# Optimization experiments

Hardware: AMD Instinct MI355X
Metric: run time of the kernel (lower is better)

The kernel has to match this reference:

```python
import jax, jax.numpy as jnp
import numpy as np

N = 500_000          # num nodes
K = 3                # neighbors per star subgraph = graphlet_size - 1
E = N * K            # one subgraph per node -> directed (center, nbr) edges
L = 2                # hop_neighbor
FD = 2               # final_dim = 2**pqc_dim
H = 64               # hidden_dim
NC = 8               # num_classes
NIN = 16             # node_input_dim
EIN = 8              # edge_input_dim


def _lin(k, i, o):
    # torch.nn.Linear-style init scale
    return jax.random.normal(k, (i, o), jnp.float32) * (1.0 / np.sqrt(i))


def setup_inputs() -> dict:
    key = jax.random.key(0)
    ks = jax.random.split(key, 32)
    node_feat = jax.random.normal(ks[0], (N, NIN), jnp.float32)
    edge_attr = jax.random.normal(ks[1], (E, EIN), jnp.float32)
    # edge e = (center, neighbor); centers grouped: edges 3i..3i+2 belong to node i
    centers = jnp.repeat(jnp.arange(N, dtype=jnp.int32), K)
    neighbors = jax.random.randint(ks[2], (E,), 0, N, dtype=jnp.int32)
    edge_index = jnp.stack([centers, neighbors])  # [2, E]
    batch = jnp.zeros((N,), jnp.int32)
    msg_W1 = jnp.stack([_lin(ks[6 + i], 2 * FD, H) for i in range(L)])
    msg_W2 = jnp.stack([_lin(ks[8 + i], H, FD) for i in range(L)])
    upd_W1 = jnp.stack([_lin(ks[10 + i], 2 * FD, H) for i in range(L)])
    upd_W2 = jnp.stack([_lin(ks[12 + i], H, FD) for i in range(L)])
    return dict(
        node_feat=node_feat, edge_attr=edge_attr, edge_index=edge_index, batch=batch,
        Wn=_lin(ks[3], NIN, FD), bn=jnp.zeros((FD,), jnp.float32),
        We=_lin(ks[4], EIN, FD), be=jnp.zeros((FD,), jnp.float32),
        msg_W1=msg_W1, msg_b1=jnp.zeros((L, H), jnp.float32),
        msg_W2=msg_W2, msg_b2=jnp.zeros((L, FD), jnp.float32),
        upd_W1=upd_W1, upd_b1=jnp.zeros((L, H), jnp.float32),
        upd_W2=upd_W2, upd_b2=jnp.zeros((L, FD), jnp.float32),
        fin_W1=_lin(ks[14], FD, H), fin_b1=jnp.zeros((H,), jnp.float32),
        fin_W2=_lin(ks[15], H, NC), fin_b2=jnp.zeros((NC,), jnp.float32),
    )


def _leaky(x):
    return jnp.where(x >= 0, x, 0.1 * x)


def _mlp(x, W1, b1, W2, b2):
    # MLP([din, 64, dout], act=LeakyReLU(0.1)); dropout inactive at eval
    return _leaky(x @ W1 + b1) @ W2 + b2


def reference(node_feat, edge_attr, edge_index, batch, Wn, bn, We, be,
              msg_W1, msg_b1, msg_W2, msg_b2, upd_W1, upd_b1, upd_W2, upd_b2,
              fin_W1, fin_b1, fin_W2, fin_b2):
    ctr = edge_index[0]  # [E] center of each star edge
    nbr = edge_index[1]  # [E] neighbor
    h = node_feat @ Wn + bn      # [N, FD] input_node projection
    e = edge_attr @ We + be      # [E, FD] input_edge projection (fixed across layers)
    for l in range(L):
        # message over each (center, neighbor) edge: concat(edge_feat, nbr_feat)
        msg = _mlp(jnp.concatenate([e, h[nbr]], axis=1),
                   msg_W1[l], msg_b1[l], msg_W2[l], msg_b2[l])  # [E, FD]
        aggr = jax.ops.segment_sum(msg, ctr, num_segments=N)    # [N, FD]
        new = _mlp(jnp.concatenate([h, aggr], axis=1),
                   upd_W1[l], upd_b1[l], upd_W2[l], upd_b2[l])  # [N, FD]
        h = jax.nn.relu(h + new)  # updates_node[center] += new_center; then ReLU
    return _mlp(h, fin_W1, fin_b1, fin_W2, fin_b2)  # [N, NC]
```

## Files before the change

kernel.cpp:

```cpp
#include <hip/hip_runtime.h>

#define NN 500000
#define KK 3
#define EE (NN * KK)
#define HH 64
#define NC 8
#define NIN 16
#define EIN 8

typedef __attribute__((ext_vector_type(2))) _Float16 h2;
typedef __attribute__((ext_vector_type(2)))  float sf2;
typedef __attribute__((ext_vector_type(8)))  float sf8;
typedef __attribute__((ext_vector_type(16))) float sf16;

using pk_t = decltype(__builtin_amdgcn_cvt_pkrtz(0.f, 0.f));

__device__ __forceinline__ sf2 sload2(const float* p) {
    sf2 r; asm("s_load_dwordx2 %0, %1, 0x0" : "=s"(r) : "s"(p)); return r;
}
__device__ __forceinline__ sf8 sload8(const float* p) {
    sf8 r; asm("s_load_dwordx8 %0, %1, 0x0" : "=s"(r) : "s"(p)); return r;
}
__device__ __forceinline__ sf16 sload16(const float* p) {
    sf16 r; asm("s_load_dwordx16 %0, %1, 0x0" : "=s"(r) : "s"(p)); return r;
}
#define SWAIT1(a)         asm volatile("s_waitcnt lgkmcnt(0)" : "+s"(a))
#define SWAIT2(a,b)       asm volatile("s_waitcnt lgkmcnt(0)" : "+s"(a),"+s"(b))
#define SWAIT3(a,b,c)     asm volatile("s_waitcnt lgkmcnt(0)" : "+s"(a),"+s"(b),"+s"(c))
#define SWAIT4(a,b,c,d)   asm volatile("s_waitcnt lgkmcnt(0)" : "+s"(a),"+s"(b),"+s"(c),"+s"(d))
#define SWAIT5(a,b,c,d,e) asm volatile("s_waitcnt lgkmcnt(0)" : "+s"(a),"+s"(b),"+s"(c),"+s"(d),"+s"(e))

#if __has_builtin(__builtin_elementwise_fma)
#define PKFMA(a,b,c) __builtin_elementwise_fma((a),(b),(c))
#else
#define PKFMA(a,b,c) ((a)*(b)+(c))
#endif

__device__ __forceinline__ h2 bch2(float f)        { return __builtin_bit_cast(h2, f); }
__device__ __forceinline__ h2 bch2u(unsigned int u){ return __builtin_bit_cast(h2, u); }
__device__ __forceinline__ h2 dup16(float f) {
    return __builtin_bit_cast(h2, __builtin_amdgcn_cvt_pkrtz(f, f));
}
__device__ __forceinline__ unsigned int pkrtz_u(float a, float b) {
    return __builtin_bit_cast(unsigned int, __builtin_amdgcn_cvt_pkrtz(a, b));
}
__device__ __forceinline__ h2 splat_lo(unsigned int u) {
    h2 p = bch2u(u); h2 r; r.x = p.x; r.y = p.x; return r;
}
__device__ __forceinline__ h2 splat_hi(unsigned int u) {
    h2 p = bch2u(u); h2 r; r.x = p.y; r.y = p.y; return r;
}
__device__ __forceinline__ float lo_f32(unsigned int u) { return (float)bch2u(u).x; }
__device__ __forceinline__ float hi_f32(unsigned int u) { return (float)bch2u(u).y; }

__device__ __forceinline__ float fdot2(h2 a, h2 b, float c) {
#if __has_builtin(__builtin_amdgcn_fdot2)
    return __builtin_amdgcn_fdot2(__builtin_bit_cast(pk_t, a),
                                  __builtin_bit_cast(pk_t, b), c, false);
#else
    return c + (float)a.x * (float)b.x + (float)a.y * (float)b.y;
#endif
}
__device__ __forceinline__ h2 lk2(h2 x) {
    h2 c = {(_Float16)0.1f, (_Float16)0.1f};
    return __builtin_elementwise_max(x, x * c);
}
__device__ __forceinline__ float pack2(float a, float b) {
    h2 v; v.x = (_Float16)a; v.y = (_Float16)b;
    return __builtin_bit_cast(float, v);
}

__global__ __launch_bounds__(256) void prep_kernel(
    const float* __restrict__ node_feat, const float* __restrict__ edge_attr,
    const float* __restrict__ Wn, const float* __restrict__ bn,
    const float* __restrict__ We, const float* __restrict__ be,
    unsigned int* __restrict__ hp, unsigned int* __restrict__ ep,
    const float* __restrict__ msgW1, const float* __restrict__ msgb1, const float* __restrict__ msgW2,
    const float* __restrict__ updW1, const float* __restrict__ updb1, const float* __restrict__ updW2,
    const float* __restrict__ finW1, const float* __restrict__ finb1, const float* __restrict__ finW2,
    float* __restrict__ wpack)
{
    sf16 wn0 = sload16(Wn);
    sf16 wn1 = sload16(Wn + 16);
    sf2  bnv = sload2(bn);
    sf16 wev = sload16(We);
    sf2  bev = sload2(be);
    SWAIT5(wn0, wn1, bnv, wev, bev);

    int idx = blockIdx.x * 256 + threadIdx.x;
    if (idx < NN) {
        const float4* x4 = (const float4*)(node_feat + (size_t)idx * NIN);
        float4 v0 = x4[0], v1 = x4[1], v2 = x4[2], v3 = x4[3];
        float xs[16] = {v0.x, v0.y, v0.z, v0.w, v1.x, v1.y, v1.z, v1.w,
                        v2.x, v2.y, v2.z, v2.w, v3.x, v3.y, v3.z, v3.w};
        float a0 = bnv.x, a1 = bnv.y;
#pragma unroll
        for (int i = 0; i < 8; i++) {
            a0 = fmaf(xs[i], wn0[2 * i], a0);
            a1 = fmaf(xs[i], wn0[2 * i + 1], a1);
        }
#pragma unroll
        for (int i = 0; i < 8; i++) {
            a0 = fmaf(xs[8 + i], wn1[2 * i], a0);
            a1 = fmaf(xs[8 + i], wn1[2 * i + 1], a1);
        }
        hp[idx] = pkrtz_u(a0, a1);
    } else if (idx < NN + EE) {
        int eidx = idx - NN;
        const float4* x4 = (const float4*)(edge_attr + (size_t)eidx * EIN);
        float4 v0 = x4[0], v1 = x4[1];
        float xs[8] = {v0.x, v0.y, v0.z, v0.w, v1.x, v1.y, v1.z, v1.w};
        float a0 = bev.x, a1 = bev.y;
#pragma unroll
        for (int i = 0; i < 8; i++) {
            a0 = fmaf(xs[i], wev[2 * i], a0);
            a1 = fmaf(xs[i], wev[2 * i + 1], a1);
        }
        ep[eidx] = pkrtz_u(a0, a1);
    }

    if (blockIdx.x == 0) {
        int t = threadIdx.x;
        if (t < 32) {
            int l = t >> 4, which = (t >> 3) & 1, c = t & 7;
            const float* W1 = (which ? updW1 : msgW1) + l * 4 * HH;
            const float* b1 = (which ? updb1 : msgb1) + l * HH;
            const float* W2 = (which ? updW2 : msgW2) + l * 2 * HH;
            float* dst = wpack + (l * 2 + which) * 256 + c * 32;
            int j0 = c * 8;
            for (int r = 0; r < 4; r++)
                for (int p = 0; p < 4; p++)
                    dst[r * 4 + p] = pack2(W1[r * HH + j0 + 2 * p], W1[r * HH + j0 + 2 * p + 1]);
            for (int p = 0; p < 4; p++) {
                dst[16 + p] = pack2(b1[j0 + 2 * p], b1[j0 + 2 * p + 1]);
                dst[20 + p] = pack2(W2[(j0 + 2 * p) * 2 + 0], W2[(j0 + 2 * p + 1) * 2 + 0]);
                dst[24 + p] = pack2(W2[(j0 + 2 * p) * 2 + 1], W2[(j0 + 2 * p + 1) * 2 + 1]);
                dst[28 + p] = 0.0f;
            }
        } else if (t < 40) {
            int c = t - 32, j0 = c * 8;
            float* dst = wpack + 1024 + c * 48;
            for (int p = 0; p < 4; p++) {
                dst[p]      = pack2(finW1[j0 + 2 * p],      finW1[j0 + 2 * p + 1]);
                dst[4 + p]  = pack2(finW1[HH + j0 + 2 * p], finW1[HH + j0 + 2 * p + 1]);
                dst[8 + p]  = pack2(finb1[j0 + 2 * p],      finb1[j0 + 2 * p + 1]);
                dst[12 + p] = 0.0f;
            }
            for (int jp = 0; jp < 4; jp++)
                for (int cc = 0; cc < NC; cc++)
                    dst[16 + jp * 8 + cc] = pack2(finW2[(j0 + 2 * jp) * NC + cc],
                                                  finW2[(j0 + 2 * jp + 1) * NC + cc]);
        }
    }
}

template<bool FINAL>
__global__ __launch_bounds__(256) void layer_kernel(
    const unsigned int* __restrict__ hp_in, const unsigned int* __restrict__ eP,
    const int* __restrict__ nbr,
    const float* __restrict__ mblk, const float* __restrict__ mb2,
    const float* __restrict__ ublk, const float* __restrict__ ub2,
    unsigned int* __restrict__ hp_out,
    const float* __restrict__ fblk, const float* __restrict__ fb2,
    float* __restrict__ out)
{
    int i = blockIdx.x * 256 + threadIdx.x;
    if (i >= NN) return;

    sf2 mb2v = sload2(mb2);
    sf2 ub2v = sload2(ub2);
    SWAIT2(mb2v, ub2v);

    unsigned int hO = hp_in[i];
    int base = i * KK;
    int n0 = nbr[base + 0], n1 = nbr[base + 1], n2 = nbr[base + 2];
    unsigned int g0 = hp_in[n0], g1 = hp_in[n1], g2 = hp_in[n2];
    unsigned int e0 = eP[base + 0], e1 = eP[base + 1], e2 = eP[base + 2];

    h2 e0x = splat_lo(e0), e0y = splat_hi(e0);
    h2 e1x = splat_lo(e1), e1y = splat_hi(e1);
    h2 e2x = splat_lo(e2), e2y = splat_hi(e2);
    h2 n0x = splat_lo(g0), n0y = splat_hi(g0);
    h2 n1x = splat_lo(g1), n1y = splat_hi(g1);
    h2 n2x = splat_lo(g2), n2y = splat_hi(g2);

    float a0 = 3.0f * mb2v.x, a1 = 3.0f * mb2v.y;
#pragma unroll 1
    for (int c = 0; c < 8; c += 2) {
        sf16 A0 = sload16(mblk + c * 32);
        sf16 B0 = sload16(mblk + c * 32 + 16);
        sf16 A1 = sload16(mblk + c * 32 + 32);
        sf16 B1 = sload16(mblk + c * 32 + 48);
        SWAIT4(A0, B0, A1, B1);
#pragma unroll
        for (int half = 0; half < 2; half++) {
            const sf16& A = half ? A1 : A0;
            const sf16& B = half ? B1 : B0;
#pragma unroll
            for (int jp = 0; jp < 4; jp++) {
                h2 w0 = bch2(A[jp]), w1 = bch2(A[4 + jp]);
                h2 w2 = bch2(A[8 + jp]), w3 = bch2(A[12 + jp]);
                h2 bb = bch2(B[jp]);
                h2 t0 = PKFMA(e0x, w0, PKFMA(e0y, w1, PKFMA(n0x, w2, PKFMA(n0y, w3, bb))));
                h2 t1 = PKFMA(e1x, w0, PKFMA(e1y, w1, PKFMA(n1x, w2, PKFMA(n1y, w3, bb))));
                h2 t2 = PKFMA(e2x, w0, PKFMA(e2y, w1, PKFMA(n2x, w2, PKFMA(n2y, w3, bb))));
                h2 ts = lk2(t0) + lk2(t1) + lk2(t2);
                a0 = fdot2(ts, bch2(B[4 + jp]), a0);
                a1 = fdot2(ts, bch2(B[8 + jp]), a1);
            }
        }
    }

    h2 hx = splat_lo(hO), hy = splat_hi(hO);
    h2 ax = dup16(a0), ay = dup16(a1);
    float u0 = ub2v.x, u1 = ub2v.y;
#pragma unroll 1
    for (int c = 0; c < 8; c += 2) {
        sf16 A0 = sload16(ublk + c * 32);
        sf16 B0 = sload16(ublk + c * 32 + 16);
        sf16 A1 = sload16(ublk + c * 32 + 32);
        sf16 B1 = sload16(ublk + c * 32 + 48);
        SWAIT4(A0, B0, A1, B1);
#pragma unroll
        for (int half = 0; half < 2; half++) {
            const sf16& A = half ? A1 : A0;
            const sf16& B = half ? B1 : B0;
#pragma unroll
            for (int jp = 0; jp < 4; jp++) {
                h2 tt = PKFMA(hx, bch2(A[jp]),
                        PKFMA(hy, bch2(A[4 + jp]),
                        PKFMA(ax, bch2(A[8 + jp]),
                        PKFMA(ay, bch2(A[12 + jp]), bch2(B[jp])))));
                tt = lk2(tt);
                u0 = fdot2(tt, bch2(B[4 + jp]), u0);
                u1 = fdot2(tt, bch2(B[8 + jp]), u1);
            }
        }
    }
    float nh0 = fmaxf(lo_f32(hO) + u0, 0.0f);
    float nh1 = fmaxf(hi_f32(hO) + u1, 0.0f);

    if constexpr (!FINAL) {
        hp_out[i] = pkrtz_u(nh0, nh1);
    } else {
        sf8 fb2v = sload8(fb2);
        SWAIT1(fb2v);
        float o[NC];
#pragma unroll
        for (int cc = 0; cc < NC; cc++) o[cc] = fb2v[cc];
        h2 nx = dup16(nh0), ny = dup16(nh1);
#pragma unroll 1
        for (int c = 0; c < 8; c++) {
            sf16 A = sload16(fblk + c * 48);
            sf16 B = sload16(fblk + c * 48 + 16);
            sf16 C = sload16(fblk + c * 48 + 32);
            SWAIT3(A, B, C);
#pragma unroll
            for (int jp = 0; jp < 4; jp++) {
                h2 w1a = bch2(A[jp]), w1b = bch2(A[4 + jp]), bb = bch2(A[8 + jp]);
                h2 tt = lk2(PKFMA(nx, w1a, PKFMA(ny, w1b, bb)));
#pragma unroll
                for (int cc = 0; cc < NC; cc++) {
                    float w = (jp < 2) ? B[(jp & 1) * 8 + cc] : C[(jp & 1) * 8 + cc];
                    o[cc] = fdot2(tt, bch2(w), o[cc]);
                }
            }
        }
        float4* op = (float4*)(out + (size_t)i * NC);
        op[0] = make_float4(o[0], o[1], o[2], o[3]);
        op[1] = make_float4(o[4], o[5], o[6], o[7]);
    }
}

extern "C" void kernel_launch(void* const* d_in, const int* in_sizes, int n_in,
                              void* d_out, int out_size, void* d_ws, size_t ws_size,
                              hipStream_t stream) {
    const float* node_feat = (const float*)d_in[0];
    const float* edge_attr = (const float*)d_in[1];
    const int* edge_index = (const int*)d_in[2];
    const float* Wn = (const float*)d_in[4];
    const float* bn = (const float*)d_in[5];
    const float* We = (const float*)d_in[6];
    const float* be = (const float*)d_in[7];
    const float* msgW1 = (const float*)d_in[8];
    const float* msgb1 = (const float*)d_in[9];
    const float* msgW2 = (const float*)d_in[10];
    const float* msgb2 = (const float*)d_in[11];
    const float* updW1 = (const float*)d_in[12];
    const float* updb1 = (const float*)d_in[13];
    const float* updW2 = (const float*)d_in[14];
    const float* updb2 = (const float*)d_in[15];
    const float* finW1 = (const float*)d_in[16];
    const float* finb1 = (const float*)d_in[17];
    const float* finW2 = (const float*)d_in[18];
    const float* finb2 = (const float*)d_in[19];
    float* out = (float*)d_out;

    const int* nbr = edge_index + EE;

    char* ws = (char*)d_ws;
    unsigned int* hA = (unsigned int*)ws;
    unsigned int* hB = (unsigned int*)(ws + (size_t)NN * 4);
    unsigned int* eP = (unsigned int*)(ws + (size_t)NN * 8);
    float* wpack = (float*)(ws + (size_t)NN * 8 + (size_t)EE * 4);

    const int threads = 256;
    int prep_grid = (NN + EE + threads - 1) / threads;
    prep_kernel<<<prep_grid, threads, 0, stream>>>(
        node_feat, edge_attr, Wn, bn, We, be, hA, eP,
        msgW1, msgb1, msgW2, updW1, updb1, updW2,
        finW1, finb1, finW2, wpack);

    int grid = (NN + threads - 1) / threads;
    layer_kernel<false><<<grid, threads, 0, stream>>>(
        hA, eP, nbr,
        wpack + 0 * 256, msgb2,
        wpack + 1 * 256, updb2,
        hB, wpack + 1024, finb2, nullptr);
    layer_kernel<true><<<grid, threads, 0, stream>>>(
        hB, eP, nbr,
        wpack + 2 * 256, msgb2 + 2,
        wpack + 3 * 256, updb2 + 2,
        nullptr, wpack + 1024, finb2, out);
}
```

Baseline: 197.4 us.

## Fuse input projections into first layer, recomputing neighbor projections

Drops the separate prep kernel and merges the node and edge input projections into the first message-passing layer. Each thread gathers raw 16-float node features for its three neighbors and re-projects them instead of reading a precomputed packed h, and it runs layer-1 MLPs in fp32. This removes one launch and the round trip of the projected h through memory. In exchange it gathers 64-byte rows instead of 4-byte ones for random neighbors and does more fp32 ALU work. Weight packing for layer 2 and the final MLP moves into block 0 of the fused kernel.

```diff
diff --git a/kernel.cpp b/kernel.cpp
--- a/kernel.cpp
+++ b/kernel.cpp
@@ -24,11 +24,11 @@
 __device__ __forceinline__ sf16 sload16(const float* p) {
     sf16 r; asm("s_load_dwordx16 %0, %1, 0x0" : "=s"(r) : "s"(p)); return r;
 }
-#define SWAIT1(a)         asm volatile("s_waitcnt lgkmcnt(0)" : "+s"(a))
-#define SWAIT2(a,b)       asm volatile("s_waitcnt lgkmcnt(0)" : "+s"(a),"+s"(b))
-#define SWAIT3(a,b,c)     asm volatile("s_waitcnt lgkmcnt(0)" : "+s"(a),"+s"(b),"+s"(c))
-#define SWAIT4(a,b,c,d)   asm volatile("s_waitcnt lgkmcnt(0)" : "+s"(a),"+s"(b),"+s"(c),"+s"(d))
-#define SWAIT5(a,b,c,d,e) asm volatile("s_waitcnt lgkmcnt(0)" : "+s"(a),"+s"(b),"+s"(c),"+s"(d),"+s"(e))
+#define SWAIT1(a)           asm volatile("s_waitcnt lgkmcnt(0)" : "+s"(a))
+#define SWAIT2(a,b)         asm volatile("s_waitcnt lgkmcnt(0)" : "+s"(a),"+s"(b))
+#define SWAIT3(a,b,c)       asm volatile("s_waitcnt lgkmcnt(0)" : "+s"(a),"+s"(b),"+s"(c))
+#define SWAIT5(a,b,c,d,e)   asm volatile("s_waitcnt lgkmcnt(0)" : "+s"(a),"+s"(b),"+s"(c),"+s"(d),"+s"(e))
+#define SWAIT6(a,b,c,d,e,f) asm volatile("s_waitcnt lgkmcnt(0)" : "+s"(a),"+s"(b),"+s"(c),"+s"(d),"+s"(e),"+s"(f))
 
 #if __has_builtin(__builtin_elementwise_fma)
 #define PKFMA(a,b,c) __builtin_elementwise_fma((a),(b),(c))
@@ -61,6 +61,7 @@
     return c + (float)a.x * (float)b.x + (float)a.y * (float)b.y;
 #endif
 }
+__device__ __forceinline__ float lky(float x)  { return fmaxf(x, 0.1f * x); }
 __device__ __forceinline__ h2 lk2(h2 x) {
     h2 c = {(_Float16)0.1f, (_Float16)0.1f};
     return __builtin_elementwise_max(x, x * c);
@@ -70,63 +71,44 @@
     return __builtin_bit_cast(float, v);
 }
 
-__global__ __launch_bounds__(256) void prep_kernel(
-    const float* __restrict__ node_feat, const float* __restrict__ edge_attr,
-    const float* __restrict__ Wn, const float* __restrict__ bn,
-    const float* __restrict__ We, const float* __restrict__ be,
-    unsigned int* __restrict__ hp, unsigned int* __restrict__ ep,
-    const float* __restrict__ msgW1, const float* __restrict__ msgb1, const float* __restrict__ msgW2,
-    const float* __restrict__ updW1, const float* __restrict__ updb1, const float* __restrict__ updW2,
-    const float* __restrict__ finW1, const float* __restrict__ finb1, const float* __restrict__ finW2,
-    float* __restrict__ wpack)
-{
-    sf16 wn0 = sload16(Wn);
-    sf16 wn1 = sload16(Wn + 16);
-    sf2  bnv = sload2(bn);
-    sf16 wev = sload16(We);
-    sf2  bev = sload2(be);
-    SWAIT5(wn0, wn1, bnv, wev, bev);
-
-    int idx = blockIdx.x * 256 + threadIdx.x;
-    if (idx < NN) {
-        const float4* x4 = (const float4*)(node_feat + (size_t)idx * NIN);
-        float4 v0 = x4[0], v1 = x4[1], v2 = x4[2], v3 = x4[3];
-        float xs[16] = {v0.x, v0.y, v0.z, v0.w, v1.x, v1.y, v1.z, v1.w,
-                        v2.x, v2.y, v2.z, v2.w, v3.x, v3.y, v3.z, v3.w};
-        float a0 = bnv.x, a1 = bnv.y;
-#pragma unroll
-        for (int i = 0; i < 8; i++) {
-            a0 = fmaf(xs[i], wn0[2 * i], a0);
-            a1 = fmaf(xs[i], wn0[2 * i + 1], a1);
-        }
-#pragma unroll
-        for (int i = 0; i < 8; i++) {
-            a0 = fmaf(xs[8 + i], wn1[2 * i], a0);
-            a1 = fmaf(xs[8 + i], wn1[2 * i + 1], a1);
-        }
-        hp[idx] = pkrtz_u(a0, a1);
-    } else if (idx < NN + EE) {
-        int eidx = idx - NN;
-        const float4* x4 = (const float4*)(edge_attr + (size_t)eidx * EIN);
-        float4 v0 = x4[0], v1 = x4[1];
-        float xs[8] = {v0.x, v0.y, v0.z, v0.w, v1.x, v1.y, v1.z, v1.w};
-        float a0 = bev.x, a1 = bev.y;
-#pragma unroll
-        for (int i = 0; i < 8; i++) {
-            a0 = fmaf(xs[i], wev[2 * i], a0);
-            a1 = fmaf(xs[i], wev[2 * i + 1], a1);
-        }
-        ep[eidx] = pkrtz_u(a0, a1);
-    }
-
+struct P1 {
+    const float *node_feat, *edge_attr; const int* nbr;
+    const float *Wn, *bn, *We, *be;
+    const float *mW1, *mb1, *mW2, *mb2, *uW1, *ub1, *uW2, *ub2;
+    const float *mW1p, *uW1p, *mb1p, *ub1p, *mW2p, *uW2p;
+    const float *fW1, *fb1, *fW2;
+    unsigned int *hp, *ep; float* wpack;
+};
+
+__device__ __forceinline__ float2 projN(const float* node_feat, int idx,
+                                        const sf16& wn0, const sf16& wn1, const sf2& bnv) {
+    const float4* x4 = (const float4*)(node_feat + (size_t)idx * NIN);
+    float4 v0 = x4[0], v1 = x4[1], v2 = x4[2], v3 = x4[3];
+    float xs[16] = {v0.x, v0.y, v0.z, v0.w, v1.x, v1.y, v1.z, v1.w,
+                    v2.x, v2.y, v2.z, v2.w, v3.x, v3.y, v3.z, v3.w};
+    float a0 = bnv.x, a1 = bnv.y;
+#pragma unroll
+    for (int i = 0; i < 8; i++) {
+        a0 = fmaf(xs[i], wn0[2 * i], a0);
+        a1 = fmaf(xs[i], wn0[2 * i + 1], a1);
+    }
+#pragma unroll
+    for (int i = 0; i < 8; i++) {
+        a0 = fmaf(xs[8 + i], wn1[2 * i], a0);
+        a1 = fmaf(xs[8 + i], wn1[2 * i + 1], a1);
+    }
+    return make_float2(a0, a1);
+}
+
+__global__ __launch_bounds__(256) void k1_kernel(P1 P) {
     if (blockIdx.x == 0) {
         int t = threadIdx.x;
-        if (t < 32) {
-            int l = t >> 4, which = (t >> 3) & 1, c = t & 7;
-            const float* W1 = (which ? updW1 : msgW1) + l * 4 * HH;
-            const float* b1 = (which ? updb1 : msgb1) + l * HH;
-            const float* W2 = (which ? updW2 : msgW2) + l * 2 * HH;
-            float* dst = wpack + (l * 2 + which) * 256 + c * 32;
+        if (t < 16) {
+            int which = t >> 3, c = t & 7;
+            const float* W1 = which ? P.uW1p : P.mW1p;
+            const float* b1 = which ? P.ub1p : P.mb1p;
+            const float* W2 = which ? P.uW2p : P.mW2p;
+            float* dst = P.wpack + (2 + which) * 256 + c * 32;
             int j0 = c * 8;
             for (int r = 0; r < 4; r++)
                 for (int p = 0; p < 4; p++)
@@ -137,30 +119,109 @@
                 dst[24 + p] = pack2(W2[(j0 + 2 * p) * 2 + 1], W2[(j0 + 2 * p + 1) * 2 + 1]);
                 dst[28 + p] = 0.0f;
             }
-        } else if (t < 40) {
-            int c = t - 32, j0 = c * 8;
-            float* dst = wpack + 1024 + c * 48;
+        } else if (t < 24) {
+            int c = t - 16, j0 = c * 8;
+            float* dst = P.wpack + 1024 + c * 48;
             for (int p = 0; p < 4; p++) {
-                dst[p]      = pack2(finW1[j0 + 2 * p],      finW1[j0 + 2 * p + 1]);
-                dst[4 + p]  = pack2(finW1[HH + j0 + 2 * p], finW1[HH + j0 + 2 * p + 1]);
-                dst[8 + p]  = pack2(finb1[j0 + 2 * p],      finb1[j0 + 2 * p + 1]);
+                dst[p]      = pack2(P.fW1[j0 + 2 * p],      P.fW1[j0 + 2 * p + 1]);
+                dst[4 + p]  = pack2(P.fW1[HH + j0 + 2 * p], P.fW1[HH + j0 + 2 * p + 1]);
+                dst[8 + p]  = pack2(P.fb1[j0 + 2 * p],      P.fb1[j0 + 2 * p + 1]);
                 dst[12 + p] = 0.0f;
             }
             for (int jp = 0; jp < 4; jp++)
                 for (int cc = 0; cc < NC; cc++)
-                    dst[16 + jp * 8 + cc] = pack2(finW2[(j0 + 2 * jp) * NC + cc],
-                                                  finW2[(j0 + 2 * jp + 1) * NC + cc]);
-        }
-    }
-}
-
-template<bool FINAL>
-__global__ __launch_bounds__(256) void layer_kernel(
+                    dst[16 + jp * 8 + cc] = pack2(P.fW2[(j0 + 2 * jp) * NC + cc],
+                                                  P.fW2[(j0 + 2 * jp + 1) * NC + cc]);
+        }
+    }
+
+    int i = blockIdx.x * 256 + threadIdx.x;
+    if (i >= NN) return;
+
+    sf16 wn0 = sload16(P.Wn);
+    sf16 wn1 = sload16(P.Wn + 16);
+    sf2  bnv = sload2(P.bn);
+    sf16 wev = sload16(P.We);
+    sf2  bev = sload2(P.be);
+    SWAIT5(wn0, wn1, bnv, wev, bev);
+
+    int base = i * KK;
+    int n0 = P.nbr[base + 0], n1 = P.nbr[base + 1], n2 = P.nbr[base + 2];
+
+    float2 hh = projN(P.node_feat, i,  wn0, wn1, bnv);
+    float2 g0 = projN(P.node_feat, n0, wn0, wn1, bnv);
+    float2 g1 = projN(P.node_feat, n1, wn0, wn1, bnv);
+    float2 g2 = projN(P.node_feat, n2, wn0, wn1, bnv);
+
+    float ex[3], ey[3];
+#pragma unroll
+    for (int k = 0; k < 3; k++) {
+        const float4* x4 = (const float4*)(P.edge_attr + (size_t)(base + k) * EIN);
+        float4 v0 = x4[0], v1 = x4[1];
+        float xs[8] = {v0.x, v0.y, v0.z, v0.w, v1.x, v1.y, v1.z, v1.w};
+        float a0 = bev.x, a1 = bev.y;
+#pragma unroll
+        for (int q = 0; q < 8; q++) {
+            a0 = fmaf(xs[q], wev[2 * q], a0);
+            a1 = fmaf(xs[q], wev[2 * q + 1], a1);
+        }
+        ex[k] = a0; ey[k] = a1;
+        P.ep[base + k] = pkrtz_u(a0, a1);
+    }
+
+    sf2 mb2v = sload2(P.mb2);
+    sf2 ub2v = sload2(P.ub2);
+    SWAIT2(mb2v, ub2v);
+
+    float a0 = 3.0f * mb2v.x, a1 = 3.0f * mb2v.y;
+#pragma unroll 1
+    for (int j0 = 0; j0 < HH; j0 += 8) {
+        sf8 w0 = sload8(P.mW1 + j0);
+        sf8 w1 = sload8(P.mW1 + HH + j0);
+        sf8 w2 = sload8(P.mW1 + 2 * HH + j0);
+        sf8 w3 = sload8(P.mW1 + 3 * HH + j0);
+        sf8 bb = sload8(P.mb1 + j0);
+        sf16 wc = sload16(P.mW2 + 2 * j0);
+        SWAIT6(w0, w1, w2, w3, bb, wc);
+#pragma unroll
+        for (int q = 0; q < 8; q++) {
+            float t0 = fmaf(ex[0], w0[q], fmaf(ey[0], w1[q], fmaf(g0.x, w2[q], fmaf(g0.y, w3[q], bb[q]))));
+            float t1 = fmaf(ex[1], w0[q], fmaf(ey[1], w1[q], fmaf(g1.x, w2[q], fmaf(g1.y, w3[q], bb[q]))));
+            float t2 = fmaf(ex[2], w0[q], fmaf(ey[2], w1[q], fmaf(g2.x, w2[q], fmaf(g2.y, w3[q], bb[q]))));
+            float ts = lky(t0) + lky(t1) + lky(t2);
+            a0 = fmaf(ts, wc[2 * q], a0);
+            a1 = fmaf(ts, wc[2 * q + 1], a1);
+        }
+    }
+
+    float u0 = ub2v.x, u1 = ub2v.y;
+#pragma unroll 1
+    for (int j0 = 0; j0 < HH; j0 += 8) {
+        sf8 w0 = sload8(P.uW1 + j0);
+        sf8 w1 = sload8(P.uW1 + HH + j0);
+        sf8 w2 = sload8(P.uW1 + 2 * HH + j0);
+        sf8 w3 = sload8(P.uW1 + 3 * HH + j0);
+        sf8 bb = sload8(P.ub1 + j0);
+        sf16 wc = sload16(P.uW2 + 2 * j0);
+        SWAIT6(w0, w1, w2, w3, bb, wc);
+#pragma unroll
+        for (int q = 0; q < 8; q++) {
+            float tt = fmaf(hh.x, w0[q], fmaf(hh.y, w1[q], fmaf(a0, w2[q], fmaf(a1, w3[q], bb[q]))));
+            tt = lky(tt);
+            u0 = fmaf(tt, wc[2 * q], u0);
+            u1 = fmaf(tt, wc[2 * q + 1], u1);
+        }
+    }
+    float nh0 = fmaxf(hh.x + u0, 0.0f);
+    float nh1 = fmaxf(hh.y + u1, 0.0f);
+    P.hp[i] = pkrtz_u(nh0, nh1);
+}
+
+__global__ __launch_bounds__(256) void k2_kernel(
     const unsigned int* __restrict__ hp_in, const unsigned int* __restrict__ eP,
     const int* __restrict__ nbr,
     const float* __restrict__ mblk, const float* __restrict__ mb2,
     const float* __restrict__ ublk, const float* __restrict__ ub2,
-    unsigned int* __restrict__ hp_out,
     const float* __restrict__ fblk, const float* __restrict__ fb2,
     float* __restrict__ out)
 {
@@ -191,7 +252,7 @@
         sf16 B0 = sload16(mblk + c * 32 + 16);
         sf16 A1 = sload16(mblk + c * 32 + 32);
         sf16 B1 = sload16(mblk + c * 32 + 48);
-        SWAIT4(A0, B0, A1, B1);
+        asm volatile("s_waitcnt lgkmcnt(0)" : "+s"(A0), "+s"(B0), "+s"(A1), "+s"(B1));
 #pragma unroll
         for (int half = 0; half < 2; half++) {
             const sf16& A = half ? A1 : A0;
@@ -220,7 +281,7 @@
         sf16 B0 = sload16(ublk + c * 32 + 16);
         sf16 A1 = sload16(ublk + c * 32 + 32);
         sf16 B1 = sload16(ublk + c * 32 + 48);
-        SWAIT4(A0, B0, A1, B1);
+        asm volatile("s_waitcnt lgkmcnt(0)" : "+s"(A0), "+s"(B0), "+s"(A1), "+s"(B1));
 #pragma unroll
         for (int half = 0; half < 2; half++) {
             const sf16& A = half ? A1 : A0;
@@ -240,36 +301,32 @@
     float nh0 = fmaxf(lo_f32(hO) + u0, 0.0f);
     float nh1 = fmaxf(hi_f32(hO) + u1, 0.0f);
 
-    if constexpr (!FINAL) {
-        hp_out[i] = pkrtz_u(nh0, nh1);
-    } else {
-        sf8 fb2v = sload8(fb2);
-        SWAIT1(fb2v);
-        float o[NC];
-#pragma unroll
-        for (int cc = 0; cc < NC; cc++) o[cc] = fb2v[cc];
-        h2 nx = dup16(nh0), ny = dup16(nh1);
-#pragma unroll 1
-        for (int c = 0; c < 8; c++) {
-            sf16 A = sload16(fblk + c * 48);
-            sf16 B = sload16(fblk + c * 48 + 16);
-            sf16 C = sload16(fblk + c * 48 + 32);
-            SWAIT3(A, B, C);
-#pragma unroll
-            for (int jp = 0; jp < 4; jp++) {
-                h2 w1a = bch2(A[jp]), w1b = bch2(A[4 + jp]), bb = bch2(A[8 + jp]);
-                h2 tt = lk2(PKFMA(nx, w1a, PKFMA(ny, w1b, bb)));
-#pragma unroll
-                for (int cc = 0; cc < NC; cc++) {
-                    float w = (jp < 2) ? B[(jp & 1) * 8 + cc] : C[(jp & 1) * 8 + cc];
-                    o[cc] = fdot2(tt, bch2(w), o[cc]);
-                }
-            }
-        }
-        float4* op = (float4*)(out + (size_t)i * NC);
-        op[0] = make_float4(o[0], o[1], o[2], o[3]);
-        op[1] = make_float4(o[4], o[5], o[6], o[7]);
-    }
+    sf8 fb2v = sload8(fb2);
+    SWAIT1(fb2v);
+    float o[NC];
+#pragma unroll
+    for (int cc = 0; cc < NC; cc++) o[cc] = fb2v[cc];
+    h2 nx = dup16(nh0), ny = dup16(nh1);
+#pragma unroll 1
+    for (int c = 0; c < 8; c++) {
+        sf16 A = sload16(fblk + c * 48);
+        sf16 B = sload16(fblk + c * 48 + 16);
+        sf16 C = sload16(fblk + c * 48 + 32);
+        SWAIT3(A, B, C);
+#pragma unroll
+        for (int jp = 0; jp < 4; jp++) {
+            h2 w1a = bch2(A[jp]), w1b = bch2(A[4 + jp]), bb = bch2(A[8 + jp]);
+            h2 tt = lk2(PKFMA(nx, w1a, PKFMA(ny, w1b, bb)));
+#pragma unroll
+            for (int cc = 0; cc < NC; cc++) {
+                float w = (jp < 2) ? B[(jp & 1) * 8 + cc] : C[(jp & 1) * 8 + cc];
+                o[cc] = fdot2(tt, bch2(w), o[cc]);
+            }
+        }
+    }
+    float4* op = (float4*)(out + (size_t)i * NC);
+    op[0] = make_float4(o[0], o[1], o[2], o[3]);
+    op[1] = make_float4(o[4], o[5], o[6], o[7]);
 }
 
 extern "C" void kernel_launch(void* const* d_in, const int* in_sizes, int n_in,
@@ -299,27 +356,26 @@
     const int* nbr = edge_index + EE;
 
     char* ws = (char*)d_ws;
-    unsigned int* hA = (unsigned int*)ws;
-    unsigned int* hB = (unsigned int*)(ws + (size_t)NN * 4);
-    unsigned int* eP = (unsigned int*)(ws + (size_t)NN * 8);
-    float* wpack = (float*)(ws + (size_t)NN * 8 + (size_t)EE * 4);
+    unsigned int* hp = (unsigned int*)ws;
+    unsigned int* ep = (unsigned int*)(ws + (size_t)NN * 4);
+    float* wpack = (float*)(ws + (size_t)NN * 4 + (size_t)EE * 4);
+
+    P1 P;
+    P.node_feat = node_feat; P.edge_attr = edge_attr; P.nbr = nbr;
+    P.Wn = Wn; P.bn = bn; P.We = We; P.be = be;
+    P.mW1 = msgW1;           P.mb1 = msgb1;           P.mW2 = msgW2;           P.mb2 = msgb2;
+    P.uW1 = updW1;           P.ub1 = updb1;           P.uW2 = updW2;           P.ub2 = updb2;
+    P.mW1p = msgW1 + 4 * HH; P.mb1p = msgb1 + HH;     P.mW2p = msgW2 + 2 * HH;
+    P.uW1p = updW1 + 4 * HH; P.ub1p = updb1 + HH;     P.uW2p = updW2 + 2 * HH;
+    P.fW1 = finW1; P.fb1 = finb1; P.fW2 = finW2;
+    P.hp = hp; P.ep = ep; P.wpack = wpack;
 
     const int threads = 256;
-    int prep_grid = (NN + EE + threads - 1) / threads;
-    prep_kernel<<<prep_grid, threads, 0, stream>>>(
-        node_feat, edge_attr, Wn, bn, We, be, hA, eP,
-        msgW1, msgb1, msgW2, updW1, updb1, updW2,
-        finW1, finb1, finW2, wpack);
-
     int grid = (NN + threads - 1) / threads;
-    layer_kernel<false><<<grid, threads, 0, stream>>>(
-        hA, eP, nbr,
-        wpack + 0 * 256, msgb2,
-        wpack + 1 * 256, updb2,
-        hB, wpack + 1024, finb2, nullptr);
-    layer_kernel<true><<<grid, threads, 0, stream>>>(
-        hB, eP, nbr,
+    k1_kernel<<<grid, threads, 0, stream>>>(P);
+    k2_kernel<<<grid, threads, 0, stream>>>(
+        hp, ep, nbr,
         wpack + 2 * 256, msgb2 + 2,
         wpack + 3 * 256, updb2 + 2,
-        nullptr, wpack + 1024, finb2, out);
-}
+        wpack + 1024, finb2, out);
+}
```

Result: slower. 213.9 us (+8.4%).
